# Kernel optimization log

Measured on AMD Instinct MI355X. Metric: run time of the kernel, lower is better.

The kernel has to match this reference:

```python
import jax, jax.numpy as jnp
import numpy as np

EMBED_DIM = 64
HIDDEN_DIM = 320
CONTEXT_DIM = 768

def setup_inputs() -> dict:
    key = jax.random.key(0)
    k1, k2, k3, k4, k5 = jax.random.split(key, 5)
    B, T, S = 4, 4096, 4096
    tokens = jax.random.normal(k1, (B, T, HIDDEN_DIM), dtype=jnp.float32)
    context = jax.random.normal(k2, (B, S, CONTEXT_DIM), dtype=jnp.float32)
    # nn.Linear(in, out, bias=False) weights, stored as [out, in] like torch
    sq = 1.0 / np.sqrt(HIDDEN_DIM)
    sk = 1.0 / np.sqrt(CONTEXT_DIM)
    Wq = jax.random.uniform(k3, (EMBED_DIM, HIDDEN_DIM), minval=-sq, maxval=sq, dtype=jnp.float32)
    Wk = jax.random.uniform(k4, (EMBED_DIM, CONTEXT_DIM), minval=-sk, maxval=sk, dtype=jnp.float32)
    Wv = jax.random.uniform(k5, (HIDDEN_DIM, CONTEXT_DIM), minval=-sk, maxval=sk, dtype=jnp.float32)
    return {"tokens": tokens, "context": context, "Wq": Wq, "Wk": Wk, "Wv": Wv}

def reference(tokens, context, Wq, Wk, Wv):
    # Q: [B,T,E], K: [B,S,E], V: [B,S,Hd]
    Q = jnp.einsum('bth,eh->bte', tokens, Wq)
    K = jnp.einsum('bsc,ec->bse', context, Wk)
    V = jnp.einsum('bsc,hc->bsh', context, Wv)
    scores = jnp.einsum('bte,bse->bts', Q, K) / np.sqrt(EMBED_DIM)
    attn = jax.nn.softmax(scores, axis=-1)  # [B,T,S] full score matrix as in original
    ctx_vecs = jnp.einsum('bts,bsh->bth', attn, V)
    return ctx_vecs
```

## Files before the change

### kernel.cpp

```cpp
#include <hip/hip_runtime.h>
#include <hip/hip_bf16.h>

typedef _Float16 half4_t  __attribute__((ext_vector_type(4)));
typedef _Float16 half8_t  __attribute__((ext_vector_type(8)));
typedef float    float4_t __attribute__((ext_vector_type(4)));

#define MFMA16x32(a, b, c) __builtin_amdgcn_mfma_f32_16x16x32_f16(a, b, c, 0, 0, 0)

__global__ __launch_bounds__(256, 4)
void wcvt_kernel(const float* __restrict__ Wq, const float* __restrict__ Wk,
                 const float* __restrict__ Wv, _Float16* __restrict__ o) {
  const int bx = blockIdx.x, t = threadIdx.x;
  const float* src;
  _Float16* dst;
  if (bx < 10) {
    int g = bx * 256 + t;
    int lane = g & 63, c = (g >> 6) & 1, rest = g >> 7;
    int nt = rest & 3, kc = rest >> 2;
    int n = nt * 16 + (lane & 15), k0 = kc * 64 + c * 32 + 8 * (lane >> 4);
    src = Wq + n * 320 + k0;
    dst = o + (size_t)g * 8;
  } else {
    int g = (bx - 10) * 256 + t;
    int lane = g & 63, c = (g >> 6) & 1, rest = g >> 7;
    int nt = rest % 24, kc = rest / 24;
    int n = nt * 16 + (lane & 15), k0 = kc * 64 + c * 32 + 8 * (lane >> 4);
    src = (nt < 4) ? (Wk + n * 768 + k0) : (Wv + (n - 64) * 768 + k0);
    dst = o + 20480 + (size_t)g * 8;
  }
  float4_t a = *(const float4_t*)(src);
  float4_t b = *(const float4_t*)(src + 4);
  half8_t h = {(_Float16)a[0], (_Float16)a[1], (_Float16)a[2], (_Float16)a[3],
               (_Float16)b[0], (_Float16)b[1], (_Float16)b[2], (_Float16)b[3]};
  *(half8_t*)dst = h;
}

__global__ __launch_bounds__(256, 2)
void proj3_kernel(const float* __restrict__ tokens, const float* __restrict__ context,
                  const _Float16* __restrict__ W16, _Float16* __restrict__ Q,
                  _Float16* __restrict__ K, _Float16* __restrict__ V) {
  __shared__ alignas(16) _Float16 Vb[320 * 72];
  const int tid = threadIdx.x, w = tid >> 6, lane = tid & 63;
  const int G = lane >> 4, l15 = lane & 15;
  const int bx = blockIdx.x;
  const _Float16* WQf = W16;
  const _Float16* WKVf = W16 + 20480;

  if (bx < 256) {
    const int m0 = bx * 64;
    const float* arow = context + (size_t)(m0 + w * 16 + l15) * 768;

    float4_t ar[4];
    auto ldA = [&](int kc) {
      ar[0] = *(const float4_t*)(arow + kc * 64 + 8 * G);
      ar[1] = *(const float4_t*)(arow + kc * 64 + 8 * G + 4);
      ar[2] = *(const float4_t*)(arow + kc * 64 + 32 + 8 * G);
      ar[3] = *(const float4_t*)(arow + kc * 64 + 36 + 8 * G);
    };

    float4_t acc[24];
#pragma unroll
    for (int nt = 0; nt < 24; ++nt) acc[nt] = {0.f, 0.f, 0.f, 0.f};

    half8_t bf[2][4][2];
    auto ldW = [&](int buf, int kc, int g) {
#pragma unroll
      for (int j = 0; j < 4; ++j)
#pragma unroll
        for (int c = 0; c < 2; ++c)
          bf[buf][j][c] = *(const half8_t*)(WKVf + ((size_t)(((kc * 24 + g * 4 + j) * 2) + c) * 64 + lane) * 8);
    };

    ldA(0);
    ldW(0, 0, 0);
    for (int kc = 0; kc < 12; ++kc) {
      half8_t af0 = {(_Float16)ar[0][0], (_Float16)ar[0][1], (_Float16)ar[0][2], (_Float16)ar[0][3],
                     (_Float16)ar[1][0], (_Float16)ar[1][1], (_Float16)ar[1][2], (_Float16)ar[1][3]};
      half8_t af1 = {(_Float16)ar[2][0], (_Float16)ar[2][1], (_Float16)ar[2][2], (_Float16)ar[2][3],
                     (_Float16)ar[3][0], (_Float16)ar[3][1], (_Float16)ar[3][2], (_Float16)ar[3][3]};
      if (kc < 11) ldA(kc + 1);
#pragma unroll
      for (int g = 0; g < 6; ++g) {
        if (g < 5) ldW((g + 1) & 1, kc, g + 1);
        else if (kc < 11) ldW(0, kc + 1, 0);
#pragma unroll
        for (int j = 0; j < 4; ++j) acc[g * 4 + j] = MFMA16x32(af0, bf[g & 1][j][0], acc[g * 4 + j]);
#pragma unroll
        for (int j = 0; j < 4; ++j) acc[g * 4 + j] = MFMA16x32(af1, bf[g & 1][j][1], acc[g * 4 + j]);
      }
    }

#pragma unroll
    for (int nt = 0; nt < 4; ++nt)
#pragma unroll
      for (int r = 0; r < 4; ++r)
        K[(size_t)(m0 + w * 16 + 4 * G + r) * 64 + nt * 16 + l15] = (_Float16)acc[nt][r];

#pragma unroll
    for (int nt = 4; nt < 24; ++nt) {
      half4_t h = {(_Float16)acc[nt][0], (_Float16)acc[nt][1], (_Float16)acc[nt][2], (_Float16)acc[nt][3]};
      *(half4_t*)(Vb + ((nt - 4) * 16 + l15) * 72 + w * 16 + 4 * G) = h;
    }
    __syncthreads();
#pragma unroll
    for (int rep = 0; rep < 10; ++rep) {
      int idx = w * 10 + rep;
      int c2 = idx / 20, htl = idx % 20;
      half8_t fr = *(const half8_t*)(Vb + (htl * 16 + l15) * 72 + c2 * 32 + 8 * G);
      int sg = m0 + c2 * 32;
      int b = sg >> 12, c2b = (sg & 4095) >> 5;
      *(half8_t*)(V + ((size_t)((b * 128 + c2b) * 20 + htl)) * 512 + lane * 8) = fr;
    }
  } else {
    const int m0 = (bx - 256) * 64;
    const float qsc = 0.125f * 1.44269504088896f;
    const float* arow = tokens + (size_t)(m0 + w * 16 + l15) * 320;

    float4_t ar[4];
    auto ldA = [&](int kc) {
      ar[0] = *(const float4_t*)(arow + kc * 64 + 8 * G);
      ar[1] = *(const float4_t*)(arow + kc * 64 + 8 * G + 4);
      ar[2] = *(const float4_t*)(arow + kc * 64 + 32 + 8 * G);
      ar[3] = *(const float4_t*)(arow + kc * 64 + 36 + 8 * G);
    };

    float4_t acc[4];
#pragma unroll
    for (int nt = 0; nt < 4; ++nt) acc[nt] = {0.f, 0.f, 0.f, 0.f};

    half8_t bq[2][4][2];
    auto ldWQ = [&](int buf, int kc) {
#pragma unroll
      for (int nt = 0; nt < 4; ++nt)
#pragma unroll
        for (int c = 0; c < 2; ++c)
          bq[buf][nt][c] = *(const half8_t*)(WQf + ((size_t)((kc * 4 + nt) * 2 + c) * 64 + lane) * 8);
    };

    ldA(0);
    ldWQ(0, 0);
    for (int kc = 0; kc < 5; ++kc) {
      half8_t af0 = {(_Float16)ar[0][0], (_Float16)ar[0][1], (_Float16)ar[0][2], (_Float16)ar[0][3],
                     (_Float16)ar[1][0], (_Float16)ar[1][1], (_Float16)ar[1][2], (_Float16)ar[1][3]};
      half8_t af1 = {(_Float16)ar[2][0], (_Float16)ar[2][1], (_Float16)ar[2][2], (_Float16)ar[2][3],
                     (_Float16)ar[3][0], (_Float16)ar[3][1], (_Float16)ar[3][2], (_Float16)ar[3][3]};
      if (kc < 4) { ldA(kc + 1); ldWQ((kc + 1) & 1, kc + 1); }
#pragma unroll
      for (int nt = 0; nt < 4; ++nt) acc[nt] = MFMA16x32(af0, bq[kc & 1][nt][0], acc[nt]);
#pragma unroll
      for (int nt = 0; nt < 4; ++nt) acc[nt] = MFMA16x32(af1, bq[kc & 1][nt][1], acc[nt]);
    }

#pragma unroll
    for (int nt = 0; nt < 4; ++nt)
#pragma unroll
      for (int r = 0; r < 4; ++r)
        Q[(size_t)(m0 + w * 16 + 4 * G + r) * 64 + nt * 16 + l15] = (_Float16)(acc[nt][r] * qsc);
  }
}

__global__ __launch_bounds__(512, 2)
void flash_kernel(const _Float16* __restrict__ Qg, const _Float16* __restrict__ Kg,
                  const _Float16* __restrict__ Vt, float* __restrict__ out) {
  __shared__ alignas(16) _Float16 kbuf[2][2048];
  __shared__ alignas(16) _Float16 pbuf[2][2048];
  __shared__ float larr[2][4][16];
  __shared__ float linv[64];

  const int tid = threadIdx.x, w = tid >> 6, lane = tid & 63;
  const int G = lane >> 4, l15 = lane & 15;
  const int bx = blockIdx.x;
  const int b = (bx & 7) >> 1;
  const int tblk = ((bx & 1) * 32 + (bx >> 3)) * 64;

  const bool is_pv = (w < 4);
  const int sw = w - 4;
  const int stile = sw & 1, tthalf = sw >> 1;
  const int t2 = tid & 255;
  const int s_loc = t2 >> 3, e8 = t2 & 7;
  const int kdst = ((s_loc >> 4) * 2 + (e8 >> 2)) * 512 + ((e8 & 3) * 16 + (s_loc & 15)) * 8;
  const _Float16* kg = Kg + (size_t)(b * 4096) * 64 + s_loc * 64 + e8 * 8;
  const _Float16* vt_b = Vt + (size_t)b * 1310720;

  half8_t qf[2][2];
  float la[2] = {0.f, 0.f};
  float4_t oa[4][5];
#pragma unroll
  for (int tt = 0; tt < 4; ++tt)
#pragma unroll
    for (int ht = 0; ht < 5; ++ht) oa[tt][ht] = {0.f, 0.f, 0.f, 0.f};
  half8_t vcur[5], vnxt[5];

  if (!is_pv) {
    uint4 k0 = *(const uint4*)(kg);
    uint4 k1 = *(const uint4*)(kg + 2048);
    *(uint4*)(&kbuf[0][kdst]) = k0;
    *(uint4*)(&kbuf[1][kdst]) = k1;
#pragma unroll
    for (int tt2 = 0; tt2 < 2; ++tt2) {
      int tt = tthalf * 2 + tt2;
#pragma unroll
      for (int c = 0; c < 2; ++c)
        qf[tt2][c] = *(const half8_t*)(Qg + (size_t)(b * 4096 + tblk + tt * 16 + l15) * 64 + c * 32 + 8 * G);
    }
  }
  __syncthreads();

  if (is_pv) {
#pragma unroll
    for (int ht = 0; ht < 5; ++ht)
      vcur[ht] = *(const half8_t*)(vt_b + (w * 5 + ht) * 512 + lane * 8);
  } else {
    half8_t af[2];
#pragma unroll
    for (int c = 0; c < 2; ++c)
      af[c] = *(const half8_t*)(&kbuf[0][(stile * 2 + c) * 512 + lane * 8]);
#pragma unroll
    for (int tt2 = 0; tt2 < 2; ++tt2) {
      float4_t sa = {0.f, 0.f, 0.f, 0.f};
#pragma unroll
      for (int c = 0; c < 2; ++c) sa = MFMA16x32(af[c], qf[tt2][c], sa);
      float e0 = exp2f(sa[0]), e1 = exp2f(sa[1]), e2 = exp2f(sa[2]), e3 = exp2f(sa[3]);
      la[tt2] += (e0 + e1) + (e2 + e3);
      int tt = tthalf * 2 + tt2;
      int Gp = stile * 2 + (G >> 1);
      half4_t p = {(_Float16)e0, (_Float16)e1, (_Float16)e2, (_Float16)e3};
      *(half4_t*)(&pbuf[0][tt * 512 + (Gp * 16 + l15) * 8 + 4 * (G & 1)]) = p;
    }
  }
  __syncthreads();

  for (int i = 0; i < 128; ++i) {
    if (is_pv) {
      if (i < 127) {
#pragma unroll
        for (int ht = 0; ht < 5; ++ht)
          vnxt[ht] = *(const half8_t*)(vt_b + (size_t)(i + 1) * 10240 + (w * 5 + ht) * 512 + lane * 8);
      }
      half8_t pa[4];
#pragma unroll
      for (int tt = 0; tt < 4; ++tt)
        pa[tt] = *(const half8_t*)(&pbuf[i & 1][tt * 512 + lane * 8]);
#pragma unroll
      for (int ht = 0; ht < 5; ++ht)
#pragma unroll
        for (int tt = 0; tt < 4; ++tt) oa[tt][ht] = MFMA16x32(pa[tt], vcur[ht], oa[tt][ht]);
#pragma unroll
      for (int ht = 0; ht < 5; ++ht) vcur[ht] = vnxt[ht];
    } else if (i < 127) {
      uint4 kreg;
      if (i < 126) kreg = *(const uint4*)(kg + (size_t)(i + 2) * 2048);
      half8_t af[2];
#pragma unroll
      for (int c = 0; c < 2; ++c)
        af[c] = *(const half8_t*)(&kbuf[(i + 1) & 1][(stile * 2 + c) * 512 + lane * 8]);
#pragma unroll
      for (int tt2 = 0; tt2 < 2; ++tt2) {
        float4_t sa = {0.f, 0.f, 0.f, 0.f};
#pragma unroll
        for (int c = 0; c < 2; ++c) sa = MFMA16x32(af[c], qf[tt2][c], sa);
        float e0 = exp2f(sa[0]), e1 = exp2f(sa[1]), e2 = exp2f(sa[2]), e3 = exp2f(sa[3]);
        la[tt2] += (e0 + e1) + (e2 + e3);
        int tt = tthalf * 2 + tt2;
        int Gp = stile * 2 + (G >> 1);
        half4_t p = {(_Float16)e0, (_Float16)e1, (_Float16)e2, (_Float16)e3};
        *(half4_t*)(&pbuf[(i + 1) & 1][tt * 512 + (Gp * 16 + l15) * 8 + 4 * (G & 1)]) = p;
      }
      if (i < 126) *(uint4*)(&kbuf[i & 1][kdst]) = kreg;
    }
    __syncthreads();
  }

  if (!is_pv) {
#pragma unroll
    for (int tt2 = 0; tt2 < 2; ++tt2) {
      float v = la[tt2];
      v += __shfl_xor(v, 16);
      v += __shfl_xor(v, 32);
      if (lane < 16) larr[stile][tthalf * 2 + tt2][l15] = v;
    }
  }
  __syncthreads();
  if (tid < 64) linv[tid] = 1.0f / (larr[0][tid >> 4][tid & 15] + larr[1][tid >> 4][tid & 15]);
  __syncthreads();
  if (is_pv) {
#pragma unroll
    for (int tt = 0; tt < 4; ++tt)
#pragma unroll
      for (int r = 0; r < 4; ++r) {
        float inv = linv[tt * 16 + 4 * G + r];
        size_t row = (size_t)(b * 4096 + tblk + tt * 16 + 4 * G + r) * 320;
#pragma unroll
        for (int ht = 0; ht < 5; ++ht)
          out[row + w * 80 + ht * 16 + l15] = oa[tt][ht][r] * inv;
      }
  }
}

extern "C" void kernel_launch(void* const* d_in, const int* in_sizes, int n_in,
                              void* d_out, int out_size, void* d_ws, size_t ws_size,
                              hipStream_t stream) {
  const float* tokens  = (const float*)d_in[0];
  const float* context = (const float*)d_in[1];
  const float* Wq      = (const float*)d_in[2];
  const float* Wk      = (const float*)d_in[3];
  const float* Wv      = (const float*)d_in[4];

  _Float16* Qws = (_Float16*)d_ws;
  _Float16* Kws = Qws + (size_t)1048576;
  _Float16* Vws = Kws + (size_t)1048576;

  const size_t W16_BYTES = (size_t)(20480 + 294912) * 2;
  const size_t BASE = (size_t)14 * 1024 * 1024;
  _Float16* W16 = (ws_size >= BASE + W16_BYTES)
                      ? (_Float16*)((char*)d_ws + BASE)
                      : (_Float16*)d_out;

  wcvt_kernel<<<dim3(154), 256, 0, stream>>>(Wq, Wk, Wv, W16);
  proj3_kernel<<<dim3(512), 256, 0, stream>>>(tokens, context, W16, Qws, Kws, Vws);
  flash_kernel<<<dim3(256), 512, 0, stream>>>(Qws, Kws, Vws, (float*)d_out);
}
```

Baseline: 240.1 us.

## Fuse weight conversion, projections and flash attention into one persistent kernel

Merges the three launches (weight cast, QKV projection, flash attention) into a single 256-block kernel. The phases are separated by atomic-counter grid barriers, and the counter and fp16 weights are placed in the output buffer. The projection phase now runs the K/V and Q GEMMs on different waves of the same block. The aim is to remove launch gaps and the tail effects between kernels. In exchange it relies on all 256 blocks being co-resident, uses a spin-wait barrier, and drops from two blocks per CU to one for the projection phase.

```diff
diff --git a/kernel.cpp b/kernel.cpp
--- a/kernel.cpp
+++ b/kernel.cpp
@@ -7,253 +7,219 @@
 
 #define MFMA16x32(a, b, c) __builtin_amdgcn_mfma_f32_16x16x32_f16(a, b, c, 0, 0, 0)
 
-__global__ __launch_bounds__(256, 4)
-void wcvt_kernel(const float* __restrict__ Wq, const float* __restrict__ Wk,
-                 const float* __restrict__ Wv, _Float16* __restrict__ o) {
-  const int bx = blockIdx.x, t = threadIdx.x;
-  const float* src;
-  _Float16* dst;
-  if (bx < 10) {
-    int g = bx * 256 + t;
-    int lane = g & 63, c = (g >> 6) & 1, rest = g >> 7;
-    int nt = rest & 3, kc = rest >> 2;
-    int n = nt * 16 + (lane & 15), k0 = kc * 64 + c * 32 + 8 * (lane >> 4);
-    src = Wq + n * 320 + k0;
-    dst = o + (size_t)g * 8;
-  } else {
-    int g = (bx - 10) * 256 + t;
-    int lane = g & 63, c = (g >> 6) & 1, rest = g >> 7;
-    int nt = rest % 24, kc = rest / 24;
-    int n = nt * 16 + (lane & 15), k0 = kc * 64 + c * 32 + 8 * (lane >> 4);
-    src = (nt < 4) ? (Wk + n * 768 + k0) : (Wv + (n - 64) * 768 + k0);
-    dst = o + 20480 + (size_t)g * 8;
-  }
-  float4_t a = *(const float4_t*)(src);
-  float4_t b = *(const float4_t*)(src + 4);
-  half8_t h = {(_Float16)a[0], (_Float16)a[1], (_Float16)a[2], (_Float16)a[3],
-               (_Float16)b[0], (_Float16)b[1], (_Float16)b[2], (_Float16)b[3]};
-  *(half8_t*)dst = h;
-}
-
-__global__ __launch_bounds__(256, 2)
-void proj3_kernel(const float* __restrict__ tokens, const float* __restrict__ context,
-                  const _Float16* __restrict__ W16, _Float16* __restrict__ Q,
-                  _Float16* __restrict__ K, _Float16* __restrict__ V) {
-  __shared__ alignas(16) _Float16 Vb[320 * 72];
+__global__ __launch_bounds__(512, 1)
+void fused_kernel(const float* __restrict__ tokens, const float* __restrict__ context,
+                  const float* __restrict__ Wq, const float* __restrict__ Wk,
+                  const float* __restrict__ Wv,
+                  _Float16* __restrict__ Qws, _Float16* __restrict__ Kws,
+                  _Float16* __restrict__ Vws,
+                  unsigned* __restrict__ syncp, _Float16* __restrict__ W16,
+                  float* __restrict__ out) {
+  __shared__ alignas(16) _Float16 smem[23040];
+  __shared__ float larr[2][4][16];
+  __shared__ float linv[64];
+
   const int tid = threadIdx.x, w = tid >> 6, lane = tid & 63;
   const int G = lane >> 4, l15 = lane & 15;
   const int bx = blockIdx.x;
-  const _Float16* WQf = W16;
-  const _Float16* WKVf = W16 + 20480;
-
-  if (bx < 256) {
+
+  auto gbar = [&](unsigned target) {
+    __syncthreads();
+    if (tid == 0) {
+      __threadfence();
+      atomicAdd(syncp, 1u);
+      while (atomicAdd(syncp, 0u) < target) __builtin_amdgcn_s_sleep(2);
+      __threadfence();
+    }
+    __syncthreads();
+  };
+
+  {
+    const int gtid = bx * 512 + tid;
+    if (gtid < 39424) {
+      const float* src;
+      _Float16* dst;
+      if (gtid < 2560) {
+        int g = gtid;
+        int ln = g & 63, c = (g >> 6) & 1, rest = g >> 7;
+        int nt = rest & 3, kc = rest >> 2;
+        int n = nt * 16 + (ln & 15), k0 = kc * 64 + c * 32 + 8 * (ln >> 4);
+        src = Wq + n * 320 + k0;
+        dst = W16 + (size_t)g * 8;
+      } else {
+        int g = gtid - 2560;
+        int ln = g & 63, c = (g >> 6) & 1, rest = g >> 7;
+        int nt = rest % 24, kc = rest / 24;
+        int n = nt * 16 + (ln & 15), k0 = kc * 64 + c * 32 + 8 * (ln >> 4);
+        src = (nt < 4) ? (Wk + n * 768 + k0) : (Wv + (n - 64) * 768 + k0);
+        dst = W16 + 20480 + (size_t)g * 8;
+      }
+      float4_t a = *(const float4_t*)(src);
+      float4_t b2 = *(const float4_t*)(src + 4);
+      half8_t h = {(_Float16)a[0], (_Float16)a[1], (_Float16)a[2], (_Float16)a[3],
+                   (_Float16)b2[0], (_Float16)b2[1], (_Float16)b2[2], (_Float16)b2[3]};
+      *(half8_t*)dst = h;
+    }
+  }
+  gbar(256);
+
+  {
+    _Float16* Vb = smem;
+    const _Float16* WQf = W16;
+    const _Float16* WKVf = W16 + 20480;
     const int m0 = bx * 64;
-    const float* arow = context + (size_t)(m0 + w * 16 + l15) * 768;
-
-    float4_t ar[4];
-    auto ldA = [&](int kc) {
-      ar[0] = *(const float4_t*)(arow + kc * 64 + 8 * G);
-      ar[1] = *(const float4_t*)(arow + kc * 64 + 8 * G + 4);
-      ar[2] = *(const float4_t*)(arow + kc * 64 + 32 + 8 * G);
-      ar[3] = *(const float4_t*)(arow + kc * 64 + 36 + 8 * G);
-    };
-
-    float4_t acc[24];
-#pragma unroll
-    for (int nt = 0; nt < 24; ++nt) acc[nt] = {0.f, 0.f, 0.f, 0.f};
-
-    half8_t bf[2][4][2];
-    auto ldW = [&](int buf, int kc, int g) {
-#pragma unroll
-      for (int j = 0; j < 4; ++j)
+
+    if (w < 4) {
+      const float* arow = context + (size_t)(m0 + w * 16 + l15) * 768;
+      float4_t ar[4];
+      auto ldA = [&](int kc) {
+        ar[0] = *(const float4_t*)(arow + kc * 64 + 8 * G);
+        ar[1] = *(const float4_t*)(arow + kc * 64 + 8 * G + 4);
+        ar[2] = *(const float4_t*)(arow + kc * 64 + 32 + 8 * G);
+        ar[3] = *(const float4_t*)(arow + kc * 64 + 36 + 8 * G);
+      };
+      float4_t acc[24];
+#pragma unroll
+      for (int nt = 0; nt < 24; ++nt) acc[nt] = {0.f, 0.f, 0.f, 0.f};
+      half8_t bf[2][4][2];
+      auto ldW = [&](int buf, int kc, int g) {
+#pragma unroll
+        for (int j = 0; j < 4; ++j)
+#pragma unroll
+          for (int c = 0; c < 2; ++c)
+            bf[buf][j][c] = *(const half8_t*)(WKVf + ((size_t)(((kc * 24 + g * 4 + j) * 2) + c) * 64 + lane) * 8);
+      };
+      ldA(0);
+      ldW(0, 0, 0);
+      for (int kc = 0; kc < 12; ++kc) {
+        half8_t af0 = {(_Float16)ar[0][0], (_Float16)ar[0][1], (_Float16)ar[0][2], (_Float16)ar[0][3],
+                       (_Float16)ar[1][0], (_Float16)ar[1][1], (_Float16)ar[1][2], (_Float16)ar[1][3]};
+        half8_t af1 = {(_Float16)ar[2][0], (_Float16)ar[2][1], (_Float16)ar[2][2], (_Float16)ar[2][3],
+                       (_Float16)ar[3][0], (_Float16)ar[3][1], (_Float16)ar[3][2], (_Float16)ar[3][3]};
+        if (kc < 11) ldA(kc + 1);
+#pragma unroll
+        for (int g = 0; g < 6; ++g) {
+          if (g < 5) ldW((g + 1) & 1, kc, g + 1);
+          else if (kc < 11) ldW(0, kc + 1, 0);
+#pragma unroll
+          for (int j = 0; j < 4; ++j) acc[g * 4 + j] = MFMA16x32(af0, bf[g & 1][j][0], acc[g * 4 + j]);
+#pragma unroll
+          for (int j = 0; j < 4; ++j) acc[g * 4 + j] = MFMA16x32(af1, bf[g & 1][j][1], acc[g * 4 + j]);
+        }
+      }
+#pragma unroll
+      for (int nt = 0; nt < 4; ++nt)
+#pragma unroll
+        for (int r = 0; r < 4; ++r)
+          Kws[(size_t)(m0 + w * 16 + 4 * G + r) * 64 + nt * 16 + l15] = (_Float16)acc[nt][r];
+#pragma unroll
+      for (int nt = 4; nt < 24; ++nt) {
+        half4_t h = {(_Float16)acc[nt][0], (_Float16)acc[nt][1], (_Float16)acc[nt][2], (_Float16)acc[nt][3]};
+        *(half4_t*)(Vb + ((nt - 4) * 16 + l15) * 72 + w * 16 + 4 * G) = h;
+      }
+    } else {
+      const int wq = w - 4;
+      const float qsc = 0.125f * 1.44269504088896f;
+      const float* arow = tokens + (size_t)(m0 + wq * 16 + l15) * 320;
+      float4_t ar[4];
+      auto ldA = [&](int kc) {
+        ar[0] = *(const float4_t*)(arow + kc * 64 + 8 * G);
+        ar[1] = *(const float4_t*)(arow + kc * 64 + 8 * G + 4);
+        ar[2] = *(const float4_t*)(arow + kc * 64 + 32 + 8 * G);
+        ar[3] = *(const float4_t*)(arow + kc * 64 + 36 + 8 * G);
+      };
+      float4_t acc[4];
+#pragma unroll
+      for (int nt = 0; nt < 4; ++nt) acc[nt] = {0.f, 0.f, 0.f, 0.f};
+      half8_t bq[2][4][2];
+      auto ldWQ = [&](int buf, int kc) {
+#pragma unroll
+        for (int nt = 0; nt < 4; ++nt)
+#pragma unroll
+          for (int c = 0; c < 2; ++c)
+            bq[buf][nt][c] = *(const half8_t*)(WQf + ((size_t)((kc * 4 + nt) * 2 + c) * 64 + lane) * 8);
+      };
+      ldA(0);
+      ldWQ(0, 0);
+      for (int kc = 0; kc < 5; ++kc) {
+        half8_t af0 = {(_Float16)ar[0][0], (_Float16)ar[0][1], (_Float16)ar[0][2], (_Float16)ar[0][3],
+                       (_Float16)ar[1][0], (_Float16)ar[1][1], (_Float16)ar[1][2], (_Float16)ar[1][3]};
+        half8_t af1 = {(_Float16)ar[2][0], (_Float16)ar[2][1], (_Float16)ar[2][2], (_Float16)ar[2][3],
+                       (_Float16)ar[3][0], (_Float16)ar[3][1], (_Float16)ar[3][2], (_Float16)ar[3][3]};
+        if (kc < 4) { ldA(kc + 1); ldWQ((kc + 1) & 1, kc + 1); }
+#pragma unroll
+        for (int nt = 0; nt < 4; ++nt) acc[nt] = MFMA16x32(af0, bq[kc & 1][nt][0], acc[nt]);
+#pragma unroll
+        for (int nt = 0; nt < 4; ++nt) acc[nt] = MFMA16x32(af1, bq[kc & 1][nt][1], acc[nt]);
+      }
+#pragma unroll
+      for (int nt = 0; nt < 4; ++nt)
+#pragma unroll
+        for (int r = 0; r < 4; ++r)
+          Qws[(size_t)(m0 + wq * 16 + 4 * G + r) * 64 + nt * 16 + l15] = (_Float16)(acc[nt][r] * qsc);
+    }
+    __syncthreads();
+    if (w < 4) {
+#pragma unroll
+      for (int rep = 0; rep < 10; ++rep) {
+        int idx = w * 10 + rep;
+        int c2 = idx / 20, htl = idx % 20;
+        half8_t fr = *(const half8_t*)(Vb + (htl * 16 + l15) * 72 + c2 * 32 + 8 * G);
+        int sg = m0 + c2 * 32;
+        int b = sg >> 12, c2b = (sg & 4095) >> 5;
+        *(half8_t*)(Vws + ((size_t)((b * 128 + c2b) * 20 + htl)) * 512 + lane * 8) = fr;
+      }
+    }
+  }
+  gbar(512);
+
+  {
+    _Float16* kb = smem;
+    _Float16* pb = smem + 4096;
+    const int b = (bx & 7) >> 1;
+    const int tblk = ((bx & 1) * 32 + (bx >> 3)) * 64;
+    const bool is_pv = (w < 4);
+    const int sw = w - 4;
+    const int stile = sw & 1, tthalf = sw >> 1;
+    const int t2 = tid & 255;
+    const int s_loc = t2 >> 3, e8 = t2 & 7;
+    const int kdst = ((s_loc >> 4) * 2 + (e8 >> 2)) * 512 + ((e8 & 3) * 16 + (s_loc & 15)) * 8;
+    const _Float16* kg = Kws + (size_t)(b * 4096) * 64 + s_loc * 64 + e8 * 8;
+    const _Float16* vt_b = Vws + (size_t)b * 1310720;
+
+    half8_t qf[2][2];
+    float la[2] = {0.f, 0.f};
+    float4_t oa[4][5];
+#pragma unroll
+    for (int tt = 0; tt < 4; ++tt)
+#pragma unroll
+      for (int ht = 0; ht < 5; ++ht) oa[tt][ht] = {0.f, 0.f, 0.f, 0.f};
+    half8_t vcur[5], vnxt[5];
+
+    if (!is_pv) {
+      uint4 k0 = *(const uint4*)(kg);
+      uint4 k1 = *(const uint4*)(kg + 2048);
+      *(uint4*)(&kb[kdst]) = k0;
+      *(uint4*)(&kb[2048 + kdst]) = k1;
+#pragma unroll
+      for (int tt2 = 0; tt2 < 2; ++tt2) {
+        int tt = tthalf * 2 + tt2;
 #pragma unroll
         for (int c = 0; c < 2; ++c)
-          bf[buf][j][c] = *(const half8_t*)(WKVf + ((size_t)(((kc * 24 + g * 4 + j) * 2) + c) * 64 + lane) * 8);
-    };
-
-    ldA(0);
-    ldW(0, 0, 0);
-    for (int kc = 0; kc < 12; ++kc) {
-      half8_t af0 = {(_Float16)ar[0][0], (_Float16)ar[0][1], (_Float16)ar[0][2], (_Float16)ar[0][3],
-                     (_Float16)ar[1][0], (_Float16)ar[1][1], (_Float16)ar[1][2], (_Float16)ar[1][3]};
-      half8_t af1 = {(_Float16)ar[2][0], (_Float16)ar[2][1], (_Float16)ar[2][2], (_Float16)ar[2][3],
-                     (_Float16)ar[3][0], (_Float16)ar[3][1], (_Float16)ar[3][2], (_Float16)ar[3][3]};
-      if (kc < 11) ldA(kc + 1);
-#pragma unroll
-      for (int g = 0; g < 6; ++g) {
-        if (g < 5) ldW((g + 1) & 1, kc, g + 1);
-        else if (kc < 11) ldW(0, kc + 1, 0);
-#pragma unroll
-        for (int j = 0; j < 4; ++j) acc[g * 4 + j] = MFMA16x32(af0, bf[g & 1][j][0], acc[g * 4 + j]);
-#pragma unroll
-        for (int j = 0; j < 4; ++j) acc[g * 4 + j] = MFMA16x32(af1, bf[g & 1][j][1], acc[g * 4 + j]);
-      }
-    }
-
-#pragma unroll
-    for (int nt = 0; nt < 4; ++nt)
-#pragma unroll
-      for (int r = 0; r < 4; ++r)
-        K[(size_t)(m0 + w * 16 + 4 * G + r) * 64 + nt * 16 + l15] = (_Float16)acc[nt][r];
-
-#pragma unroll
-    for (int nt = 4; nt < 24; ++nt) {
-      half4_t h = {(_Float16)acc[nt][0], (_Float16)acc[nt][1], (_Float16)acc[nt][2], (_Float16)acc[nt][3]};
-      *(half4_t*)(Vb + ((nt - 4) * 16 + l15) * 72 + w * 16 + 4 * G) = h;
-    }
-    __syncthreads();
-#pragma unroll
-    for (int rep = 0; rep < 10; ++rep) {
-      int idx = w * 10 + rep;
-      int c2 = idx / 20, htl = idx % 20;
-      half8_t fr = *(const half8_t*)(Vb + (htl * 16 + l15) * 72 + c2 * 32 + 8 * G);
-      int sg = m0 + c2 * 32;
-      int b = sg >> 12, c2b = (sg & 4095) >> 5;
-      *(half8_t*)(V + ((size_t)((b * 128 + c2b) * 20 + htl)) * 512 + lane * 8) = fr;
-    }
-  } else {
-    const int m0 = (bx - 256) * 64;
-    const float qsc = 0.125f * 1.44269504088896f;
-    const float* arow = tokens + (size_t)(m0 + w * 16 + l15) * 320;
-
-    float4_t ar[4];
-    auto ldA = [&](int kc) {
-      ar[0] = *(const float4_t*)(arow + kc * 64 + 8 * G);
-      ar[1] = *(const float4_t*)(arow + kc * 64 + 8 * G + 4);
-      ar[2] = *(const float4_t*)(arow + kc * 64 + 32 + 8 * G);
-      ar[3] = *(const float4_t*)(arow + kc * 64 + 36 + 8 * G);
-    };
-
-    float4_t acc[4];
-#pragma unroll
-    for (int nt = 0; nt < 4; ++nt) acc[nt] = {0.f, 0.f, 0.f, 0.f};
-
-    half8_t bq[2][4][2];
-    auto ldWQ = [&](int buf, int kc) {
-#pragma unroll
-      for (int nt = 0; nt < 4; ++nt)
-#pragma unroll
-        for (int c = 0; c < 2; ++c)
-          bq[buf][nt][c] = *(const half8_t*)(WQf + ((size_t)((kc * 4 + nt) * 2 + c) * 64 + lane) * 8);
-    };
-
-    ldA(0);
-    ldWQ(0, 0);
-    for (int kc = 0; kc < 5; ++kc) {
-      half8_t af0 = {(_Float16)ar[0][0], (_Float16)ar[0][1], (_Float16)ar[0][2], (_Float16)ar[0][3],
-                     (_Float16)ar[1][0], (_Float16)ar[1][1], (_Float16)ar[1][2], (_Float16)ar[1][3]};
-      half8_t af1 = {(_Float16)ar[2][0], (_Float16)ar[2][1], (_Float16)ar[2][2], (_Float16)ar[2][3],
-                     (_Float16)ar[3][0], (_Float16)ar[3][1], (_Float16)ar[3][2], (_Float16)ar[3][3]};
-      if (kc < 4) { ldA(kc + 1); ldWQ((kc + 1) & 1, kc + 1); }
-#pragma unroll
-      for (int nt = 0; nt < 4; ++nt) acc[nt] = MFMA16x32(af0, bq[kc & 1][nt][0], acc[nt]);
-#pragma unroll
-      for (int nt = 0; nt < 4; ++nt) acc[nt] = MFMA16x32(af1, bq[kc & 1][nt][1], acc[nt]);
-    }
-
-#pragma unroll
-    for (int nt = 0; nt < 4; ++nt)
-#pragma unroll
-      for (int r = 0; r < 4; ++r)
-        Q[(size_t)(m0 + w * 16 + 4 * G + r) * 64 + nt * 16 + l15] = (_Float16)(acc[nt][r] * qsc);
-  }
-}
-
-__global__ __launch_bounds__(512, 2)
-void flash_kernel(const _Float16* __restrict__ Qg, const _Float16* __restrict__ Kg,
-                  const _Float16* __restrict__ Vt, float* __restrict__ out) {
-  __shared__ alignas(16) _Float16 kbuf[2][2048];
-  __shared__ alignas(16) _Float16 pbuf[2][2048];
-  __shared__ float larr[2][4][16];
-  __shared__ float linv[64];
-
-  const int tid = threadIdx.x, w = tid >> 6, lane = tid & 63;
-  const int G = lane >> 4, l15 = lane & 15;
-  const int bx = blockIdx.x;
-  const int b = (bx & 7) >> 1;
-  const int tblk = ((bx & 1) * 32 + (bx >> 3)) * 64;
-
-  const bool is_pv = (w < 4);
-  const int sw = w - 4;
-  const int stile = sw & 1, tthalf = sw >> 1;
-  const int t2 = tid & 255;
-  const int s_loc = t2 >> 3, e8 = t2 & 7;
-  const int kdst = ((s_loc >> 4) * 2 + (e8 >> 2)) * 512 + ((e8 & 3) * 16 + (s_loc & 15)) * 8;
-  const _Float16* kg = Kg + (size_t)(b * 4096) * 64 + s_loc * 64 + e8 * 8;
-  const _Float16* vt_b = Vt + (size_t)b * 1310720;
-
-  half8_t qf[2][2];
-  float la[2] = {0.f, 0.f};
-  float4_t oa[4][5];
-#pragma unroll
-  for (int tt = 0; tt < 4; ++tt)
-#pragma unroll
-    for (int ht = 0; ht < 5; ++ht) oa[tt][ht] = {0.f, 0.f, 0.f, 0.f};
-  half8_t vcur[5], vnxt[5];
-
-  if (!is_pv) {
-    uint4 k0 = *(const uint4*)(kg);
-    uint4 k1 = *(const uint4*)(kg + 2048);
-    *(uint4*)(&kbuf[0][kdst]) = k0;
-    *(uint4*)(&kbuf[1][kdst]) = k1;
-#pragma unroll
-    for (int tt2 = 0; tt2 < 2; ++tt2) {
-      int tt = tthalf * 2 + tt2;
+          qf[tt2][c] = *(const half8_t*)(Qws + (size_t)(b * 4096 + tblk + tt * 16 + l15) * 64 + c * 32 + 8 * G);
+      }
+    }
+    __syncthreads();
+
+    if (is_pv) {
+#pragma unroll
+      for (int ht = 0; ht < 5; ++ht)
+        vcur[ht] = *(const half8_t*)(vt_b + (w * 5 + ht) * 512 + lane * 8);
+    } else {
+      half8_t af[2];
 #pragma unroll
       for (int c = 0; c < 2; ++c)
-        qf[tt2][c] = *(const half8_t*)(Qg + (size_t)(b * 4096 + tblk + tt * 16 + l15) * 64 + c * 32 + 8 * G);
-    }
-  }
-  __syncthreads();
-
-  if (is_pv) {
-#pragma unroll
-    for (int ht = 0; ht < 5; ++ht)
-      vcur[ht] = *(const half8_t*)(vt_b + (w * 5 + ht) * 512 + lane * 8);
-  } else {
-    half8_t af[2];
-#pragma unroll
-    for (int c = 0; c < 2; ++c)
-      af[c] = *(const half8_t*)(&kbuf[0][(stile * 2 + c) * 512 + lane * 8]);
-#pragma unroll
-    for (int tt2 = 0; tt2 < 2; ++tt2) {
-      float4_t sa = {0.f, 0.f, 0.f, 0.f};
-#pragma unroll
-      for (int c = 0; c < 2; ++c) sa = MFMA16x32(af[c], qf[tt2][c], sa);
-      float e0 = exp2f(sa[0]), e1 = exp2f(sa[1]), e2 = exp2f(sa[2]), e3 = exp2f(sa[3]);
-      la[tt2] += (e0 + e1) + (e2 + e3);
-      int tt = tthalf * 2 + tt2;
-      int Gp = stile * 2 + (G >> 1);
-      half4_t p = {(_Float16)e0, (_Float16)e1, (_Float16)e2, (_Float16)e3};
-      *(half4_t*)(&pbuf[0][tt * 512 + (Gp * 16 + l15) * 8 + 4 * (G & 1)]) = p;
-    }
-  }
-  __syncthreads();
-
-  for (int i = 0; i < 128; ++i) {
-    if (is_pv) {
-      if (i < 127) {
-#pragma unroll
-        for (int ht = 0; ht < 5; ++ht)
-          vnxt[ht] = *(const half8_t*)(vt_b + (size_t)(i + 1) * 10240 + (w * 5 + ht) * 512 + lane * 8);
-      }
-      half8_t pa[4];
-#pragma unroll
-      for (int tt = 0; tt < 4; ++tt)
-        pa[tt] = *(const half8_t*)(&pbuf[i & 1][tt * 512 + lane * 8]);
-#pragma unroll
-      for (int ht = 0; ht < 5; ++ht)
-#pragma unroll
-        for (int tt = 0; tt < 4; ++tt) oa[tt][ht] = MFMA16x32(pa[tt], vcur[ht], oa[tt][ht]);
-#pragma unroll
-      for (int ht = 0; ht < 5; ++ht) vcur[ht] = vnxt[ht];
-    } else if (i < 127) {
-      uint4 kreg;
-      if (i < 126) kreg = *(const uint4*)(kg + (size_t)(i + 2) * 2048);
-      half8_t af[2];
-#pragma unroll
-      for (int c = 0; c < 2; ++c)
-        af[c] = *(const half8_t*)(&kbuf[(i + 1) & 1][(stile * 2 + c) * 512 + lane * 8]);
+        af[c] = *(const half8_t*)(&kb[(stile * 2 + c) * 512 + lane * 8]);
 #pragma unroll
       for (int tt2 = 0; tt2 < 2; ++tt2) {
         float4_t sa = {0.f, 0.f, 0.f, 0.f};
@@ -264,36 +230,76 @@
         int tt = tthalf * 2 + tt2;
         int Gp = stile * 2 + (G >> 1);
         half4_t p = {(_Float16)e0, (_Float16)e1, (_Float16)e2, (_Float16)e3};
-        *(half4_t*)(&pbuf[(i + 1) & 1][tt * 512 + (Gp * 16 + l15) * 8 + 4 * (G & 1)]) = p;
-      }
-      if (i < 126) *(uint4*)(&kbuf[i & 1][kdst]) = kreg;
-    }
-    __syncthreads();
-  }
-
-  if (!is_pv) {
-#pragma unroll
-    for (int tt2 = 0; tt2 < 2; ++tt2) {
-      float v = la[tt2];
-      v += __shfl_xor(v, 16);
-      v += __shfl_xor(v, 32);
-      if (lane < 16) larr[stile][tthalf * 2 + tt2][l15] = v;
-    }
-  }
-  __syncthreads();
-  if (tid < 64) linv[tid] = 1.0f / (larr[0][tid >> 4][tid & 15] + larr[1][tid >> 4][tid & 15]);
-  __syncthreads();
-  if (is_pv) {
-#pragma unroll
-    for (int tt = 0; tt < 4; ++tt)
-#pragma unroll
-      for (int r = 0; r < 4; ++r) {
-        float inv = linv[tt * 16 + 4 * G + r];
-        size_t row = (size_t)(b * 4096 + tblk + tt * 16 + 4 * G + r) * 320;
+        *(half4_t*)(&pb[tt * 512 + (Gp * 16 + l15) * 8 + 4 * (G & 1)]) = p;
+      }
+    }
+    __syncthreads();
+
+    for (int i = 0; i < 128; ++i) {
+      if (is_pv) {
+        if (i < 127) {
+#pragma unroll
+          for (int ht = 0; ht < 5; ++ht)
+            vnxt[ht] = *(const half8_t*)(vt_b + (size_t)(i + 1) * 10240 + (w * 5 + ht) * 512 + lane * 8);
+        }
+        half8_t pa[4];
+#pragma unroll
+        for (int tt = 0; tt < 4; ++tt)
+          pa[tt] = *(const half8_t*)(&pb[(i & 1) * 2048 + tt * 512 + lane * 8]);
 #pragma unroll
         for (int ht = 0; ht < 5; ++ht)
-          out[row + w * 80 + ht * 16 + l15] = oa[tt][ht][r] * inv;
-      }
+#pragma unroll
+          for (int tt = 0; tt < 4; ++tt) oa[tt][ht] = MFMA16x32(pa[tt], vcur[ht], oa[tt][ht]);
+#pragma unroll
+        for (int ht = 0; ht < 5; ++ht) vcur[ht] = vnxt[ht];
+      } else if (i < 127) {
+        uint4 kreg;
+        if (i < 126) kreg = *(const uint4*)(kg + (size_t)(i + 2) * 2048);
+        half8_t af[2];
+#pragma unroll
+        for (int c = 0; c < 2; ++c)
+          af[c] = *(const half8_t*)(&kb[((i + 1) & 1) * 2048 + (stile * 2 + c) * 512 + lane * 8]);
+#pragma unroll
+        for (int tt2 = 0; tt2 < 2; ++tt2) {
+          float4_t sa = {0.f, 0.f, 0.f, 0.f};
+#pragma unroll
+          for (int c = 0; c < 2; ++c) sa = MFMA16x32(af[c], qf[tt2][c], sa);
+          float e0 = exp2f(sa[0]), e1 = exp2f(sa[1]), e2 = exp2f(sa[2]), e3 = exp2f(sa[3]);
+          la[tt2] += (e0 + e1) + (e2 + e3);
+          int tt = tthalf * 2 + tt2;
+          int Gp = stile * 2 + (G >> 1);
+          half4_t p = {(_Float16)e0, (_Float16)e1, (_Float16)e2, (_Float16)e3};
+          *(half4_t*)(&pb[((i + 1) & 1) * 2048 + tt * 512 + (Gp * 16 + l15) * 8 + 4 * (G & 1)]) = p;
+        }
+        if (i < 126) *(uint4*)(&kb[(i & 1) * 2048 + kdst]) = kreg;
+      }
+      __syncthreads();
+    }
+
+    if (!is_pv) {
+#pragma unroll
+      for (int tt2 = 0; tt2 < 2; ++tt2) {
+        float v = la[tt2];
+        v += __shfl_xor(v, 16);
+        v += __shfl_xor(v, 32);
+        if (lane < 16) larr[stile][tthalf * 2 + tt2][l15] = v;
+      }
+    }
+    __syncthreads();
+    if (tid < 64) linv[tid] = 1.0f / (larr[0][tid >> 4][tid & 15] + larr[1][tid >> 4][tid & 15]);
+    __syncthreads();
+    if (is_pv) {
+#pragma unroll
+      for (int tt = 0; tt < 4; ++tt)
+#pragma unroll
+        for (int r = 0; r < 4; ++r) {
+          float inv = linv[tt * 16 + 4 * G + r];
+          size_t row = (size_t)(b * 4096 + tblk + tt * 16 + 4 * G + r) * 320;
+#pragma unroll
+          for (int ht = 0; ht < 5; ++ht)
+            out[row + w * 80 + ht * 16 + l15] = oa[tt][ht][r] * inv;
+        }
+    }
   }
 }
 
@@ -310,13 +316,10 @@
   _Float16* Kws = Qws + (size_t)1048576;
   _Float16* Vws = Kws + (size_t)1048576;
 
-  const size_t W16_BYTES = (size_t)(20480 + 294912) * 2;
-  const size_t BASE = (size_t)14 * 1024 * 1024;
-  _Float16* W16 = (ws_size >= BASE + W16_BYTES)
-                      ? (_Float16*)((char*)d_ws + BASE)
-                      : (_Float16*)d_out;
-
-  wcvt_kernel<<<dim3(154), 256, 0, stream>>>(Wq, Wk, Wv, W16);
-  proj3_kernel<<<dim3(512), 256, 0, stream>>>(tokens, context, W16, Qws, Kws, Vws);
-  flash_kernel<<<dim3(256), 512, 0, stream>>>(Qws, Kws, Vws, (float*)d_out);
+  unsigned* syncp = (unsigned*)d_out;
+  _Float16* W16  = (_Float16*)((char*)d_out + 256);
+
+  hipMemsetAsync(d_out, 0, 8, stream);
+  fused_kernel<<<dim3(256), dim3(512), 0, stream>>>(
+      tokens, context, Wq, Wk, Wv, Qws, Kws, Vws, syncp, W16, (float*)d_out);
 }
```

Result: slower. 281.6 us (+17.2%).
